# Kernel optimization log

Measured on AMD Instinct MI355X. Metric: run time of the kernel, lower is better.

The kernel has to match this reference:

```python
import jax, jax.numpy as jnp
import numpy as np

N = 50000
E = 800000
IN_DIM = 128
F_NUM = 64
OUT_DIM = 16


def gcn_norm(edge_index, edge_weight, num_nodes):
    # add self loops with fill value 1.0 (improved=False), then symmetric norm
    e = edge_index.shape[1]
    w = jnp.ones((e,), jnp.float32) if edge_weight is None else edge_weight
    loop = jnp.arange(num_nodes, dtype=edge_index.dtype)
    row = jnp.concatenate([edge_index[0], loop])
    col = jnp.concatenate([edge_index[1], loop])
    w = jnp.concatenate([w, jnp.ones((num_nodes,), jnp.float32)])
    deg = jax.ops.segment_sum(w, col, num_segments=num_nodes)
    dis = jnp.where(deg > 0, jax.lax.rsqrt(jnp.where(deg > 0, deg, 1.0)), 0.0)
    norm = dis[row] * w * dis[col]
    return row, col, norm


def dgconv(x, edge_index, edge_weight, num_nodes):
    row, col, norm = gcn_norm(edge_index, edge_weight, num_nodes)
    # gather -> scale -> scatter-add
    msg = norm[:, None] * x[row]          # [E+N, F]
    return jax.ops.segment_sum(msg, col, num_segments=num_nodes)


def setup_inputs() -> dict:
    key = jax.random.key(0)
    ks = jax.random.split(key, 12)
    x = jax.random.normal(ks[0], (N, IN_DIM), jnp.float32)
    edge_index = jax.random.randint(ks[1], (2, E), 0, N, jnp.int64 if jax.config.jax_enable_x64 else jnp.int32)
    edge_in = jax.random.randint(ks[2], (2, E), 0, N, edge_index.dtype)
    edge_out = jax.random.randint(ks[3], (2, E), 0, N, edge_index.dtype)
    in_w = jax.random.uniform(ks[4], (E,), jnp.float32)
    out_w = jax.random.uniform(ks[5], (E,), jnp.float32)
    lin1_w = jax.random.normal(ks[6], (F_NUM, IN_DIM), jnp.float32) / np.sqrt(IN_DIM)
    lin2_w = jax.random.normal(ks[7], (F_NUM, 3 * F_NUM), jnp.float32) / np.sqrt(3 * F_NUM)
    bias1 = jnp.zeros((1, F_NUM), jnp.float32)
    bias2 = jnp.zeros((1, F_NUM), jnp.float32)
    conv_w = jax.random.normal(ks[8], (OUT_DIM, 3 * F_NUM), jnp.float32) / np.sqrt(3 * F_NUM)
    conv_b = jnp.zeros((OUT_DIM,), jnp.float32)
    return {"x": x, "edge_index": edge_index, "edge_in": edge_in, "edge_out": edge_out,
            "in_w": in_w, "out_w": out_w, "lin1_w": lin1_w, "lin2_w": lin2_w,
            "bias1": bias1, "bias2": bias2, "conv_w": conv_w, "conv_b": conv_b}


def reference(x, edge_index, edge_in, edge_out, in_w, out_w,
              lin1_w, lin2_w, bias1, bias2, conv_w, conv_b):
    n = x.shape[0]
    h = x @ lin1_w.T                                          # [N, F]
    h1 = dgconv(h, edge_index, None, n) + bias1
    h2 = dgconv(h, edge_in, in_w, n) + bias1
    h3 = dgconv(h, edge_out, out_w, n) + bias1
    h = jax.nn.relu(jnp.concatenate([h1, h2, h3], axis=-1))   # [N, 3F]
    h = h @ lin2_w.T                                          # [N, F]
    h1 = dgconv(h, edge_index, None, n) + bias2
    h2 = dgconv(h, edge_in, in_w, n) + bias2
    h3 = dgconv(h, edge_out, out_w, n) + bias2
    h = jax.nn.relu(jnp.concatenate([h1, h2, h3], axis=-1))   # [N, 3F]
    # Conv1d(kernel_size=1) == pointwise linear over channels
    logits = h @ conv_w.T + conv_b                            # [N, out_dim]
    return jax.nn.log_softmax(logits, axis=1)
```

## Files before the change

### kernel.cpp

```cpp
#include <hip/hip_runtime.h>
#include <hip/hip_fp16.h>
#include <math.h>

#define FDIM 64
#define CATDIM 192
#define CH 8192
#define MAXNB 1024
#define SCTILE 1024


__global__ __launch_bounds__(256) void k_chist(const int* __restrict__ ei0,
                                               const int* __restrict__ ei1,
                                               const int* __restrict__ ei2,
                                               int* __restrict__ bh,
                                               int NB, int nchunks, int E) {
    __shared__ int hist[MAXNB];
    const int c = blockIdx.x, g = blockIdx.y, tid = threadIdx.x;
    const int* dest = (g == 0 ? ei0 : g == 1 ? ei1 : ei2) + E;

    for (int i = tid; i < NB; i += 256) hist[i] = 0;
    __syncthreads();

    const int lo = c * CH, hi = min(E, lo + CH);
    for (int i = lo + tid; i < hi; i += 256) atomicAdd(&hist[dest[i] >> 6], 1);
    __syncthreads();

    for (int i = tid; i < NB; i += 256)
        bh[((size_t)g * NB + i) * nchunks + c] = hist[i];
}


__global__ __launch_bounds__(256) void k_scan_a(const int* __restrict__ bh,
                                                int* __restrict__ bsum,
                                                int L, int nblkS) {
    __shared__ int s[256];
    const int b = blockIdx.x, g = blockIdx.y, tid = threadIdx.x;
    const int* data = bh + (size_t)g * L;
    const int base = b * SCTILE + tid * 4;
    int v = 0;
#pragma unroll
    for (int j = 0; j < 4; ++j) {
        int idx = base + j;
        if (idx < L) v += data[idx];
    }
    s[tid] = v;
    __syncthreads();
    for (int d = 128; d > 0; d >>= 1) {
        if (tid < d) s[tid] += s[tid + d];
        __syncthreads();
    }
    if (tid == 0) bsum[g * nblkS + b] = s[0];
}

__global__ __launch_bounds__(256) void k_scan_b(int* __restrict__ bsum, int nblkS) {
    __shared__ int s[256];
    const int g = blockIdx.x, tid = threadIdx.x;
    int v = (tid < nblkS) ? bsum[g * nblkS + tid] : 0;
    s[tid] = v;
    __syncthreads();
    for (int d = 1; d < 256; d <<= 1) {
        int t = (tid >= d) ? s[tid - d] : 0;
        __syncthreads();
        s[tid] += t;
        __syncthreads();
    }
    if (tid < nblkS) bsum[g * nblkS + tid] = s[tid] - v;
}

__global__ __launch_bounds__(256) void k_scan_c(int* __restrict__ bh,
                                                const int* __restrict__ bsum,
                                                int L, int nblkS) {
    __shared__ int s[256];
    const int b = blockIdx.x, g = blockIdx.y, tid = threadIdx.x;
    int* data = bh + (size_t)g * L;
    const int base = b * SCTILE + tid * 4;

    int e0 = 0, e1 = 0, e2 = 0, e3 = 0;
    if (base + 0 < L) e0 = data[base + 0];
    if (base + 1 < L) e1 = data[base + 1];
    if (base + 2 < L) e2 = data[base + 2];
    if (base + 3 < L) e3 = data[base + 3];
    int tot = e0 + e1 + e2 + e3;
    s[tid] = tot;
    __syncthreads();
    for (int d = 1; d < 256; d <<= 1) {
        int t = (tid >= d) ? s[tid - d] : 0;
        __syncthreads();
        s[tid] += t;
        __syncthreads();
    }
    int run = bsum[g * nblkS + b] + s[tid] - tot;
    if (base + 0 < L) { data[base + 0] = run; run += e0; }
    if (base + 1 < L) { data[base + 1] = run; run += e1; }
    if (base + 2 < L) { data[base + 2] = run; run += e2; }
    if (base + 3 < L) { data[base + 3] = run; run += e3; }
}


__global__ void k_bbase(const int* __restrict__ bh, int* __restrict__ bbase,
                        int NB, int nchunks, int E) {
    int i = blockIdx.x * blockDim.x + threadIdx.x;
    if (i >= 3 * NB) return;
    int g = i / NB, b = i - g * NB;
    bbase[g * (NB + 1) + b] = bh[((size_t)g * NB + b) * nchunks];
    if (b == 0) bbase[g * (NB + 1) + NB] = E;
}


__global__ __launch_bounds__(256) void k_cfill(const int* __restrict__ ei0,
                                               const int* __restrict__ ei1,
                                               const int* __restrict__ ei2,
                                               const float* __restrict__ w1,
                                               const float* __restrict__ w2,
                                               const int* __restrict__ bh,
                                               int2* __restrict__ barr,
                                               int NB, int nchunks, int E) {
    __shared__ int cur[MAXNB];
    const int c = blockIdx.x, g = blockIdx.y, tid = threadIdx.x;
    const int* e = (g == 0 ? ei0 : g == 1 ? ei1 : ei2);
    const float* w = (g == 1 ? w1 : w2);
    const int* srcp = e;
    const int* dest = e + E;
    int2* bout = barr + (size_t)g * E;

    for (int i = tid; i < NB; i += 256)
        cur[i] = bh[((size_t)g * NB + i) * nchunks + c];
    __syncthreads();

    const int lo = c * CH, hi = min(E, lo + CH);
    for (int i = lo + tid; i < hi; i += 256) {
        int d = dest[i];
        int slot = atomicAdd(&cur[d >> 6], 1);
        float wv = (g == 0) ? 0.f : w[i];
        bout[slot] = make_int2(srcp[i] | ((d & 63) << 16), __float_as_int(wv));
    }
}


__global__ __launch_bounds__(256) void k_bsort(const int2* __restrict__ barr,
                                               const int* __restrict__ bbase,
                                               unsigned* __restrict__ csr,
                                               int* __restrict__ rowptr,
                                               float* __restrict__ dis,
                                               int N, int E, int NB) {
    __shared__ int hist[64];
    __shared__ float wsum[64];
    __shared__ int cur[64];
    __shared__ int sc[64];

    const int b = blockIdx.x, g = blockIdx.y, tid = threadIdx.x;
    const int2* bin = barr + (size_t)g * E;
    const int beg = bbase[g * (NB + 1) + b];
    const int end = bbase[g * (NB + 1) + b + 1];

    if (tid < 64) { hist[tid] = 0; wsum[tid] = 1.0f; }
    __syncthreads();

    for (int t = beg + tid; t < end; t += 256) {
        int2 p = bin[t];
        int dl = (p.x >> 16) & 63;
        atomicAdd(&hist[dl], 1);
        if (g) atomicAdd(&wsum[dl], __int_as_float(p.y));
    }
    __syncthreads();

    if (tid < 64) sc[tid] = hist[tid];
    __syncthreads();
    for (int d = 1; d < 64; d <<= 1) {
        int t = 0;
        if (tid < 64 && tid >= d) t = sc[tid - d];
        __syncthreads();
        if (tid < 64) sc[tid] += t;
        __syncthreads();
    }
    if (tid < 64) {
        int excl = sc[tid] - hist[tid];
        cur[tid] = excl;
        int node = b * 64 + tid;
        if (node < N) {
            rowptr[g * (N + 1) + node] = beg + excl;
            float s = g ? wsum[tid] : (1.0f + (float)hist[tid]);
            dis[g * N + node] = rsqrtf(s);
        }
    }
    if (b == NB - 1 && tid == 0) rowptr[g * (N + 1) + N] = end;
    __syncthreads();

    for (int t = beg + tid; t < end; t += 256) {
        int2 p = bin[t];
        int dl = (p.x >> 16) & 63;
        int pos = atomicAdd(&cur[dl], 1);
        unsigned short wb = __half_as_ushort(__float2half(__int_as_float(p.y)));
        csr[(size_t)g * E + beg + pos] = (unsigned)(p.x & 0xFFFF) | ((unsigned)wb << 16);
    }
}


__global__ void k_scale(unsigned* __restrict__ csr, const float* __restrict__ dis,
                        int N, int E) {
    int idx = blockIdx.x * blockDim.x + threadIdx.x;
    if (idx >= 3 * E) return;
    int g = idx >= 2 * E ? 2 : (idx >= E ? 1 : 0);
    unsigned u = csr[idx];
    int s = u & 0xFFFFu;
    float d = dis[g * N + s];
    float v = (g == 0) ? d
                       : __half2float(__ushort_as_half((unsigned short)(u >> 16))) * d;
    csr[idx] = (u & 0xFFFFu) |
               ((unsigned)__half_as_ushort(__float2half(v)) << 16);
}


template <typename T> __device__ inline float4 load4f(const T* p);
template <> __device__ inline float4 load4f<float>(const float* p) {
    return *reinterpret_cast<const float4*>(p);
}
template <> __device__ inline float4 load4f<__half>(const __half* p) {
    __half2 a = *reinterpret_cast<const __half2*>(p);
    __half2 b = *reinterpret_cast<const __half2*>(p + 2);
    float2 fa = __half22float2(a), fb = __half22float2(b);
    return make_float4(fa.x, fa.y, fb.x, fb.y);
}

template <int K, typename TA>
__global__ __launch_bounds__(256) void k_gemm(const TA* __restrict__ A,
                                              const float* __restrict__ W,
                                              __half* __restrict__ out, int n) {
    __shared__ float wt[K * 65];
    __shared__ float xs[64 * 36];

    const int tid = threadIdx.x;
    const int n0 = blockIdx.x * 64;

    for (int idx = tid; idx < FDIM * K; idx += 256) {
        int fr = idx / K;
        int kr = idx - fr * K;
        wt[kr * 65 + fr] = W[idx];
    }

    const int f = tid & 63;
    const int q = tid >> 6;
    float acc[16];
#pragma unroll
    for (int j = 0; j < 16; ++j) acc[j] = 0.f;

    for (int kc = 0; kc < K; kc += 32) {
        __syncthreads();
#pragma unroll
        for (int u = tid; u < 512; u += 256) {
            int node = u >> 3;
            int k4 = u & 7;
            int gn = n0 + node;
            float4 a = make_float4(0.f, 0.f, 0.f, 0.f);
            if (gn < n) a = load4f(&A[(size_t)gn * K + kc + k4 * 4]);
            *reinterpret_cast<float4*>(&xs[node * 36 + k4 * 4]) = a;
        }
        __syncthreads();

#pragma unroll
        for (int kk = 0; kk < 32; kk += 4) {
            float w0 = wt[(kc + kk + 0) * 65 + f];
            float w1 = wt[(kc + kk + 1) * 65 + f];
            float w2 = wt[(kc + kk + 2) * 65 + f];
            float w3 = wt[(kc + kk + 3) * 65 + f];
#pragma unroll
            for (int jj = 0; jj < 16; ++jj) {
                int j = jj * 4 + q;
                float4 av = *reinterpret_cast<const float4*>(&xs[j * 36 + kk]);
                acc[jj] = fmaf(av.x, w0, fmaf(av.y, w1, fmaf(av.z, w2, fmaf(av.w, w3, acc[jj]))));
            }
        }
    }

#pragma unroll
    for (int jj = 0; jj < 16; ++jj) {
        int node = n0 + jj * 4 + q;
        if (node < n) out[(size_t)node * FDIM + f] = __float2half(acc[jj]);
    }
}


__global__ __launch_bounds__(256) void k_gather(const __half* __restrict__ h,
                                                const float* __restrict__ dis,
                                                const int* __restrict__ rowptr,
                                                const unsigned* __restrict__ csr,
                                                const float* __restrict__ bias,
                                                __half* __restrict__ cat,
                                                int N, int E) {
    int i = blockIdx.x * 4 + (threadIdx.x >> 6);
    if (i >= N) return;
    const int lane = threadIdx.x & 63;

    const float hv = __half2float(h[(size_t)i * FDIM + lane]);
    const float b = bias[lane];

#pragma unroll
    for (int g = 0; g < 3; ++g) {
        const int* rp = rowptr + g * (N + 1);
        const unsigned* cg = csr + (size_t)g * E;
        const int beg = __builtin_amdgcn_readfirstlane(rp[i]);
        const int end = __builtin_amdgcn_readfirstlane(rp[i + 1]);
        float dg = dis[g * N + i];

        float acc0 = 0.f, acc1 = 0.f, acc2 = 0.f, acc3 = 0.f;
        float acc4 = 0.f, acc5 = 0.f, acc6 = 0.f, acc7 = 0.f;
        int j = beg;
        for (; j + 8 <= end; j += 8) {
            unsigned u0 = cg[j + 0];
            unsigned u1 = cg[j + 1];
            unsigned u2 = cg[j + 2];
            unsigned u3 = cg[j + 3];
            unsigned u4 = cg[j + 4];
            unsigned u5 = cg[j + 5];
            unsigned u6 = cg[j + 6];
            unsigned u7 = cg[j + 7];
            float a0 = __half2float(h[(size_t)(u0 & 0xFFFFu) * FDIM + lane]);
            float a1 = __half2float(h[(size_t)(u1 & 0xFFFFu) * FDIM + lane]);
            float a2 = __half2float(h[(size_t)(u2 & 0xFFFFu) * FDIM + lane]);
            float a3 = __half2float(h[(size_t)(u3 & 0xFFFFu) * FDIM + lane]);
            float a4 = __half2float(h[(size_t)(u4 & 0xFFFFu) * FDIM + lane]);
            float a5 = __half2float(h[(size_t)(u5 & 0xFFFFu) * FDIM + lane]);
            float a6 = __half2float(h[(size_t)(u6 & 0xFFFFu) * FDIM + lane]);
            float a7 = __half2float(h[(size_t)(u7 & 0xFFFFu) * FDIM + lane]);
            acc0 = fmaf(__half2float(__ushort_as_half((unsigned short)(u0 >> 16))), a0, acc0);
            acc1 = fmaf(__half2float(__ushort_as_half((unsigned short)(u1 >> 16))), a1, acc1);
            acc2 = fmaf(__half2float(__ushort_as_half((unsigned short)(u2 >> 16))), a2, acc2);
            acc3 = fmaf(__half2float(__ushort_as_half((unsigned short)(u3 >> 16))), a3, acc3);
            acc4 = fmaf(__half2float(__ushort_as_half((unsigned short)(u4 >> 16))), a4, acc4);
            acc5 = fmaf(__half2float(__ushort_as_half((unsigned short)(u5 >> 16))), a5, acc5);
            acc6 = fmaf(__half2float(__ushort_as_half((unsigned short)(u6 >> 16))), a6, acc6);
            acc7 = fmaf(__half2float(__ushort_as_half((unsigned short)(u7 >> 16))), a7, acc7);
        }
        if (j + 4 <= end) {
            unsigned u0 = cg[j + 0];
            unsigned u1 = cg[j + 1];
            unsigned u2 = cg[j + 2];
            unsigned u3 = cg[j + 3];
            float a0 = __half2float(h[(size_t)(u0 & 0xFFFFu) * FDIM + lane]);
            float a1 = __half2float(h[(size_t)(u1 & 0xFFFFu) * FDIM + lane]);
            float a2 = __half2float(h[(size_t)(u2 & 0xFFFFu) * FDIM + lane]);
            float a3 = __half2float(h[(size_t)(u3 & 0xFFFFu) * FDIM + lane]);
            acc0 = fmaf(__half2float(__ushort_as_half((unsigned short)(u0 >> 16))), a0, acc0);
            acc1 = fmaf(__half2float(__ushort_as_half((unsigned short)(u1 >> 16))), a1, acc1);
            acc2 = fmaf(__half2float(__ushort_as_half((unsigned short)(u2 >> 16))), a2, acc2);
            acc3 = fmaf(__half2float(__ushort_as_half((unsigned short)(u3 >> 16))), a3, acc3);
            j += 4;
        }
        for (; j < end; ++j) {
            unsigned u0 = cg[j];
            float a0 = __half2float(h[(size_t)(u0 & 0xFFFFu) * FDIM + lane]);
            acc0 = fmaf(__half2float(__ushort_as_half((unsigned short)(u0 >> 16))), a0, acc0);
        }
        float outv = dg * (((acc0 + acc1) + (acc2 + acc3)) + ((acc4 + acc5) + (acc6 + acc7)))
                   + dg * dg * hv + b;
        cat[(size_t)i * CATDIM + g * FDIM + lane] = __float2half(outv > 0.f ? outv : 0.f);
    }
}


__global__ __launch_bounds__(256) void k_final(const __half* __restrict__ cat,
                                               const float* __restrict__ convw,
                                               const float* __restrict__ convb,
                                               float* __restrict__ out, int n) {
    __shared__ float wl[16 * 196];
    __shared__ float bl[16];
    const int tid = threadIdx.x;
    for (int t = tid; t < 16 * 192; t += 256) {
        int o = t / 192;
        int k = t - o * 192;
        wl[o * 196 + k] = convw[t];
    }
    if (tid < 16) bl[tid] = convb[tid];
    __syncthreads();

    const int o = tid & 15;
    const int node = blockIdx.x * 16 + (tid >> 4);
    const int nc = node < n ? node : n - 1;

    const float4* xr4 = reinterpret_cast<const float4*>(cat + (size_t)nc * CATDIM);
    const float* wr = &wl[o * 196];
    float acc = bl[o];
#pragma unroll
    for (int k8 = 0; k8 < CATDIM / 8; ++k8) {
        float4 raw = xr4[k8];
        const __half2* hp = reinterpret_cast<const __half2*>(&raw);
        float2 f0 = __half22float2(hp[0]);
        float2 f1 = __half22float2(hp[1]);
        float2 f2 = __half22float2(hp[2]);
        float2 f3 = __half22float2(hp[3]);
        const float* w8 = wr + k8 * 8;
        acc += f0.x * w8[0] + f0.y * w8[1] + f1.x * w8[2] + f1.y * w8[3] +
               f2.x * w8[4] + f2.y * w8[5] + f3.x * w8[6] + f3.y * w8[7];
    }

    float m = acc;
    m = fmaxf(m, __shfl_xor(m, 1));
    m = fmaxf(m, __shfl_xor(m, 2));
    m = fmaxf(m, __shfl_xor(m, 4));
    m = fmaxf(m, __shfl_xor(m, 8));
    float s = __expf(acc - m);
    s += __shfl_xor(s, 1);
    s += __shfl_xor(s, 2);
    s += __shfl_xor(s, 4);
    s += __shfl_xor(s, 8);
    if (node < n) out[(size_t)node * 16 + o] = acc - m - logf(s);
}


extern "C" void kernel_launch(void* const* d_in, const int* in_sizes, int n_in,
                              void* d_out, int out_size, void* d_ws, size_t ws_size,
                              hipStream_t stream) {
    const float* x      = (const float*)d_in[0];
    const int*   ei     = (const int*)d_in[1];
    const int*   e_in   = (const int*)d_in[2];
    const int*   e_out  = (const int*)d_in[3];
    const float* in_w   = (const float*)d_in[4];
    const float* out_w  = (const float*)d_in[5];
    const float* lin1_w = (const float*)d_in[6];
    const float* lin2_w = (const float*)d_in[7];
    const float* bias1  = (const float*)d_in[8];
    const float* bias2  = (const float*)d_in[9];
    const float* conv_w = (const float*)d_in[10];
    const float* conv_b = (const float*)d_in[11];
    float* out = (float*)d_out;

    const int N = in_sizes[0] / 128;
    const int E = in_sizes[1] / 2;
    const int NB = (N + 63) >> 6;
    const int nchunks = (E + CH - 1) / CH;
    const int L = NB * nchunks;
    const int nblkS = (L + SCTILE - 1) / SCTILE;

    float* ws = (float*)d_ws;
    size_t o = 0;
    float* dis    = ws + o;            o += (size_t)3 * N;
    int*   rowptr = (int*)(ws + o);    o += ((size_t)3 * (N + 1) + 1) & ~1ull;
    int*   bbase  = (int*)(ws + o);    o += ((size_t)3 * (NB + 1) + 1) & ~1ull;
    int*   bsum   = (int*)(ws + o);    o += ((size_t)3 * nblkS + 1) & ~1ull;
    int*   bh     = (int*)(ws + o);    o += ((size_t)3 * L + 3) & ~3ull;
    __half* h     = (__half*)(ws + o); o += (size_t)N * (FDIM / 2);
    o = (o + 3) & ~3ull;
    unsigned* csr = (unsigned*)(ws + o); o += (size_t)3 * E;
    o = (o + 3) & ~3ull;
    __half* cat   = (__half*)(ws + o); o += (size_t)N * (CATDIM / 2);
    int2*  barr   = (int2*)cat;

    const int B = 256;

    hipLaunchKernelGGL(k_chist, dim3(nchunks, 3), dim3(B), 0, stream, ei, e_in, e_out, bh, NB, nchunks, E);
    hipLaunchKernelGGL(k_scan_a, dim3(nblkS, 3), dim3(B), 0, stream, bh, bsum, L, nblkS);
    hipLaunchKernelGGL(k_scan_b, dim3(3), dim3(B), 0, stream, bsum, nblkS);
    hipLaunchKernelGGL(k_scan_c, dim3(nblkS, 3), dim3(B), 0, stream, bh, bsum, L, nblkS);
    hipLaunchKernelGGL(k_bbase, dim3((3 * NB + B - 1) / B), dim3(B), 0, stream, bh, bbase, NB, nchunks, E);
    hipLaunchKernelGGL(k_cfill, dim3(nchunks, 3), dim3(B), 0, stream,
                       ei, e_in, e_out, in_w, out_w, bh, barr, NB, nchunks, E);
    hipLaunchKernelGGL(k_bsort, dim3(NB, 3), dim3(B), 0, stream,
                       barr, bbase, csr, rowptr, dis, N, E, NB);
    hipLaunchKernelGGL(k_scale, dim3((3 * E + B - 1) / B), dim3(B), 0, stream, csr, dis, N, E);

    hipLaunchKernelGGL((k_gemm<128, float>), dim3((N + 63) / 64), dim3(B), 0, stream, x, lin1_w, h, N);
    hipLaunchKernelGGL(k_gather, dim3((N + 3) / 4), dim3(B), 0, stream,
                       h, dis, rowptr, csr, bias1, cat, N, E);

    hipLaunchKernelGGL((k_gemm<192, __half>), dim3((N + 63) / 64), dim3(B), 0, stream, cat, lin2_w, h, N);
    hipLaunchKernelGGL(k_gather, dim3((N + 3) / 4), dim3(B), 0, stream,
                       h, dis, rowptr, csr, bias2, cat, N, E);

    hipLaunchKernelGGL(k_final, dim3((N + 15) / 16), dim3(B), 0, stream, cat, conv_w, conv_b, out, N);
}
```

Measured before the change: 409.0 us.

## Shrink edge chunks, transpose block histograms, and fold scaling into CSR placement

New measurement: 413.7 us. No clear change (+1.1%).

```diff
diff --git a/kernel.cpp b/kernel.cpp
--- a/kernel.cpp
+++ b/kernel.cpp
@@ -4,19 +4,20 @@
 
 #define FDIM 64
 #define CATDIM 192
-#define CH 8192
+#define CH 2048
 #define MAXNB 1024
-#define SCTILE 1024
+#define SCTILE 2048
 
 
 __global__ __launch_bounds__(256) void k_chist(const int* __restrict__ ei0,
                                                const int* __restrict__ ei1,
                                                const int* __restrict__ ei2,
-                                               int* __restrict__ bh,
+                                               int* __restrict__ bhT,
                                                int NB, int nchunks, int E) {
     __shared__ int hist[MAXNB];
     const int c = blockIdx.x, g = blockIdx.y, tid = threadIdx.x;
     const int* dest = (g == 0 ? ei0 : g == 1 ? ei1 : ei2) + E;
+    const size_t L = (size_t)NB * nchunks;
 
     for (int i = tid; i < NB; i += 256) hist[i] = 0;
     __syncthreads();
@@ -26,7 +27,31 @@
     __syncthreads();
 
     for (int i = tid; i < NB; i += 256)
-        bh[((size_t)g * NB + i) * nchunks + c] = hist[i];
+        bhT[g * L + (size_t)c * NB + i] = hist[i];
+}
+
+
+__global__ __launch_bounds__(256) void k_tr(const int* __restrict__ in,
+                                            int* __restrict__ out,
+                                            int rows, int cols) {
+    __shared__ int tile[32][33];
+    const int g = blockIdx.z;
+    const int c0 = blockIdx.x * 32;
+    const int r0 = blockIdx.y * 32;
+    const int tx = threadIdx.x & 31, ty0 = threadIdx.x >> 5;
+    const size_t L = (size_t)rows * cols;
+    const int* pin = in + (size_t)g * L;
+    int* pout = out + (size_t)g * L;
+
+    for (int dy = 0; dy < 32; dy += 8) {
+        int r = r0 + ty0 + dy, c = c0 + tx;
+        tile[ty0 + dy][tx] = (r < rows && c < cols) ? pin[(size_t)r * cols + c] : 0;
+    }
+    __syncthreads();
+    for (int dy = 0; dy < 32; dy += 8) {
+        int c = c0 + ty0 + dy, r = r0 + tx;
+        if (c < cols && r < rows) pout[(size_t)c * rows + r] = tile[tx][ty0 + dy];
+    }
 }
 
 
@@ -36,10 +61,10 @@
     __shared__ int s[256];
     const int b = blockIdx.x, g = blockIdx.y, tid = threadIdx.x;
     const int* data = bh + (size_t)g * L;
-    const int base = b * SCTILE + tid * 4;
+    const int base = b * SCTILE + tid * 8;
     int v = 0;
 #pragma unroll
-    for (int j = 0; j < 4; ++j) {
+    for (int j = 0; j < 8; ++j) {
         int idx = base + j;
         if (idx < L) v += data[idx];
     }
@@ -73,14 +98,15 @@
     __shared__ int s[256];
     const int b = blockIdx.x, g = blockIdx.y, tid = threadIdx.x;
     int* data = bh + (size_t)g * L;
-    const int base = b * SCTILE + tid * 4;
-
-    int e0 = 0, e1 = 0, e2 = 0, e3 = 0;
-    if (base + 0 < L) e0 = data[base + 0];
-    if (base + 1 < L) e1 = data[base + 1];
-    if (base + 2 < L) e2 = data[base + 2];
-    if (base + 3 < L) e3 = data[base + 3];
-    int tot = e0 + e1 + e2 + e3;
+    const int base = b * SCTILE + tid * 8;
+
+    int e[8];
+    int tot = 0;
+#pragma unroll
+    for (int j = 0; j < 8; ++j) {
+        e[j] = (base + j < L) ? data[base + j] : 0;
+        tot += e[j];
+    }
     s[tid] = tot;
     __syncthreads();
     for (int d = 1; d < 256; d <<= 1) {
@@ -90,10 +116,14 @@
         __syncthreads();
     }
     int run = bsum[g * nblkS + b] + s[tid] - tot;
-    if (base + 0 < L) { data[base + 0] = run; run += e0; }
-    if (base + 1 < L) { data[base + 1] = run; run += e1; }
-    if (base + 2 < L) { data[base + 2] = run; run += e2; }
-    if (base + 3 < L) { data[base + 3] = run; run += e3; }
+#pragma unroll
+    for (int j = 0; j < 8; ++j) {
+        if (base + j < L) {
+            int v = e[j];
+            data[base + j] = run;
+            run += v;
+        }
+    }
 }
 
 
@@ -112,7 +142,7 @@
                                                const int* __restrict__ ei2,
                                                const float* __restrict__ w1,
                                                const float* __restrict__ w2,
-                                               const int* __restrict__ bh,
+                                               const int* __restrict__ bhT2,
                                                int2* __restrict__ barr,
                                                int NB, int nchunks, int E) {
     __shared__ int cur[MAXNB];
@@ -122,9 +152,10 @@
     const int* srcp = e;
     const int* dest = e + E;
     int2* bout = barr + (size_t)g * E;
+    const size_t L = (size_t)NB * nchunks;
 
     for (int i = tid; i < NB; i += 256)
-        cur[i] = bh[((size_t)g * NB + i) * nchunks + c];
+        cur[i] = bhT2[g * L + (size_t)c * NB + i];
     __syncthreads();
 
     const int lo = c * CH, hi = min(E, lo + CH);
@@ -137,15 +168,13 @@
 }
 
 
-__global__ __launch_bounds__(256) void k_bsort(const int2* __restrict__ barr,
-                                               const int* __restrict__ bbase,
-                                               unsigned* __restrict__ csr,
-                                               int* __restrict__ rowptr,
-                                               float* __restrict__ dis,
-                                               int N, int E, int NB) {
+__global__ __launch_bounds__(256) void k_deg(const int2* __restrict__ barr,
+                                             const int* __restrict__ bbase,
+                                             int* __restrict__ rowptr,
+                                             float* __restrict__ dis,
+                                             int N, int E, int NB) {
     __shared__ int hist[64];
     __shared__ float wsum[64];
-    __shared__ int cur[64];
     __shared__ int sc[64];
 
     const int b = blockIdx.x, g = blockIdx.y, tid = threadIdx.x;
@@ -174,40 +203,45 @@
         __syncthreads();
     }
     if (tid < 64) {
-        int excl = sc[tid] - hist[tid];
-        cur[tid] = excl;
         int node = b * 64 + tid;
         if (node < N) {
-            rowptr[g * (N + 1) + node] = beg + excl;
+            rowptr[g * (N + 1) + node] = beg + (sc[tid] - hist[tid]);
             float s = g ? wsum[tid] : (1.0f + (float)hist[tid]);
             dis[g * N + node] = rsqrtf(s);
         }
     }
     if (b == NB - 1 && tid == 0) rowptr[g * (N + 1) + N] = end;
+}
+
+
+__global__ __launch_bounds__(256) void k_place(const int2* __restrict__ barr,
+                                               const int* __restrict__ bbase,
+                                               const int* __restrict__ rowptr,
+                                               const float* __restrict__ dis,
+                                               unsigned* __restrict__ csr,
+                                               int N, int E, int NB) {
+    __shared__ int cur[64];
+    const int b = blockIdx.x, g = blockIdx.y, tid = threadIdx.x;
+    const int2* bin = barr + (size_t)g * E;
+    const int beg = bbase[g * (NB + 1) + b];
+    const int end = bbase[g * (NB + 1) + b + 1];
+
+    if (tid < 64) {
+        int node = b * 64 + tid;
+        cur[tid] = (node < N) ? rowptr[g * (N + 1) + node] - beg : 0;
+    }
     __syncthreads();
 
     for (int t = beg + tid; t < end; t += 256) {
         int2 p = bin[t];
         int dl = (p.x >> 16) & 63;
         int pos = atomicAdd(&cur[dl], 1);
-        unsigned short wb = __half_as_ushort(__float2half(__int_as_float(p.y)));
-        csr[(size_t)g * E + beg + pos] = (unsigned)(p.x & 0xFFFF) | ((unsigned)wb << 16);
-    }
-}
-
-
-__global__ void k_scale(unsigned* __restrict__ csr, const float* __restrict__ dis,
-                        int N, int E) {
-    int idx = blockIdx.x * blockDim.x + threadIdx.x;
-    if (idx >= 3 * E) return;
-    int g = idx >= 2 * E ? 2 : (idx >= E ? 1 : 0);
-    unsigned u = csr[idx];
-    int s = u & 0xFFFFu;
-    float d = dis[g * N + s];
-    float v = (g == 0) ? d
-                       : __half2float(__ushort_as_half((unsigned short)(u >> 16))) * d;
-    csr[idx] = (u & 0xFFFFu) |
-               ((unsigned)__half_as_ushort(__float2half(v)) << 16);
+        int src = p.x & 0xFFFF;
+        float wv = g ? __int_as_float(p.y) : 1.0f;
+        float v = wv * dis[g * N + src];
+        unsigned short wb = __half_as_ushort(__float2half(v));
+        csr[(size_t)g * E + beg + pos] = (unsigned)src | ((unsigned)wb << 16);
+    }
 }
 
 
@@ -438,6 +472,7 @@
     int*   bbase  = (int*)(ws + o);    o += ((size_t)3 * (NB + 1) + 1) & ~1ull;
     int*   bsum   = (int*)(ws + o);    o += ((size_t)3 * nblkS + 1) & ~1ull;
     int*   bh     = (int*)(ws + o);    o += ((size_t)3 * L + 3) & ~3ull;
+    int*   bhT    = (int*)(ws + o);    o += ((size_t)3 * L + 3) & ~3ull;
     __half* h     = (__half*)(ws + o); o += (size_t)N * (FDIM / 2);
     o = (o + 3) & ~3ull;
     unsigned* csr = (unsigned*)(ws + o); o += (size_t)3 * E;
@@ -447,16 +482,19 @@
 
     const int B = 256;
 
-    hipLaunchKernelGGL(k_chist, dim3(nchunks, 3), dim3(B), 0, stream, ei, e_in, e_out, bh, NB, nchunks, E);
+    hipLaunchKernelGGL(k_chist, dim3(nchunks, 3), dim3(B), 0, stream, ei, e_in, e_out, bhT, NB, nchunks, E);
+    hipLaunchKernelGGL(k_tr, dim3((NB + 31) / 32, (nchunks + 31) / 32, 3), dim3(B), 0, stream,
+                       bhT, bh, nchunks, NB);
     hipLaunchKernelGGL(k_scan_a, dim3(nblkS, 3), dim3(B), 0, stream, bh, bsum, L, nblkS);
     hipLaunchKernelGGL(k_scan_b, dim3(3), dim3(B), 0, stream, bsum, nblkS);
     hipLaunchKernelGGL(k_scan_c, dim3(nblkS, 3), dim3(B), 0, stream, bh, bsum, L, nblkS);
     hipLaunchKernelGGL(k_bbase, dim3((3 * NB + B - 1) / B), dim3(B), 0, stream, bh, bbase, NB, nchunks, E);
+    hipLaunchKernelGGL(k_tr, dim3((nchunks + 31) / 32, (NB + 31) / 32, 3), dim3(B), 0, stream,
+                       bh, bhT, NB, nchunks);
     hipLaunchKernelGGL(k_cfill, dim3(nchunks, 3), dim3(B), 0, stream,
-                       ei, e_in, e_out, in_w, out_w, bh, barr, NB, nchunks, E);
-    hipLaunchKernelGGL(k_bsort, dim3(NB, 3), dim3(B), 0, stream,
-                       barr, bbase, csr, rowptr, dis, N, E, NB);
-    hipLaunchKernelGGL(k_scale, dim3((3 * E + B - 1) / B), dim3(B), 0, stream, csr, dis, N, E);
+                       ei, e_in, e_out, in_w, out_w, bhT, barr, NB, nchunks, E);
+    hipLaunchKernelGGL(k_deg, dim3(NB, 3), dim3(B), 0, stream, barr, bbase, rowptr, dis, N, E, NB);
+    hipLaunchKernelGGL(k_place, dim3(NB, 3), dim3(B), 0, stream, barr, bbase, rowptr, dis, csr, N, E, NB);
 
     hipLaunchKernelGGL((k_gemm<128, float>), dim3((N + 63) / 64), dim3(B), 0, stream, x, lin1_w, h, N);
     hipLaunchKernelGGL(k_gather, dim3((N + 3) / 4), dim3(B), 0, stream,
```
